# Performance work log

Measured on AMD Instinct MI355X. Metric: run time of the kernel, lower is better.

The kernel has to match this reference:

```python
import jax, jax.numpy as jnp
import numpy as np

INPUT_SIZE = 4096.0
SIGMA = 3
CONF_THR = 0.8
DIST_THR = (6 * SIGMA + 2) / 2.0  # 10.0, as in DecodeSPM.__init__
KP_DIST_THR = 2.0                 # hardcoded in forward's get_spm_keypoints call
MAX_ROOTS = 256                   # fixed cap on greedy NMS iterations (padded outputs)


def setup_inputs() -> dict:
    key = jax.random.key(0)
    x = jax.random.normal(key, (1, 35, 1024, 1024), dtype=jnp.float32)
    return {"x": x}


def _decode_spm(x):
    S = x.shape[-1]
    hm = jax.nn.sigmoid(x[0, 0])      # [S, S] root-joint heatmap (pred=True)
    disp = jnp.tanh(x[0, 1:])         # [2*Kp, S, S] displacement maps
    num_kp = disp.shape[0] // 2
    z = jnp.sqrt(jnp.asarray(2.0, x.dtype)) * S  # sqrt(S^2 + S^2)

    conf = hm.reshape(-1)             # [S*S]
    ii = jnp.arange(S * S)
    ys = (ii // S).astype(x.dtype)
    xs = (ii % S).astype(x.dtype)
    # candidates below conf threshold are permanently suppressed
    scores0 = jnp.where(conf > CONF_THR, conf, -jnp.inf)

    def step(scores, _):
        idx = jnp.argmax(scores)                      # highest remaining confidence
        valid = jnp.isfinite(scores[idx])
        cx, cy = xs[idx], ys[idx]
        d2 = (xs - cx) ** 2 + (ys - cy) ** 2
        # greedy suppression: drop everything within DIST_THR (incl. chosen point)
        scores = jnp.where(d2 <= DIST_THR ** 2, -jnp.inf, scores)
        return scores, (cx, cy, valid)

    _, (cxs, cys, valids) = jax.lax.scan(step, scores0, None, length=MAX_ROOTS)

    mask = valids.astype(x.dtype)                     # [R]
    root = jnp.stack([cxs, cys], axis=-1) * mask[:, None]   # [R, 2] (x, y)

    # gather displacement values at each root location: [2*Kp, R] -> [R, Kp, 2]
    yi = cys.astype(jnp.int32)
    xi = cxs.astype(jnp.int32)
    dvals = disp[:, yi, xi].T.reshape(MAX_ROOTS, num_kp, 2)  # (dx, dy) per kp

    kp = dvals * z + root[:, None, :]                  # [R, Kp, 2]
    d = jnp.sqrt(jnp.sum((kp - root[:, None, :]) ** 2, axis=-1, keepdims=True))
    kp = jnp.where(d < KP_DIST_THR, jnp.zeros_like(kp), kp) * mask[:, None, None]

    scale = INPUT_SIZE / S
    return root * scale, kp * scale, valids


def reference(x):
    # root_joints [MAX_ROOTS, 2], keypoints [MAX_ROOTS, Kp, 2], validity mask [MAX_ROOTS]
    return _decode_spm(x)
```

## Files before the change

kernel.cpp:

```cpp
#include <hip/hip_runtime.h>
#include <math.h>


#define SS 1024
#define MAXR 256
#define NBIN 16384
#define CAP 1024
#define TARGET 768u
#define B0 0x3F4CCCCEu
#define KEYB0 0xBF4CCCCEu
#define CONFL_MAX 8
#define CELL_CAP 8

struct WS {
  unsigned int hist[NBIN];
  unsigned int dstOff[NBIN];
  unsigned int cutBits;
  unsigned int candCount;
  int nValid;
  int pad0;
  int rootX[MAXR];
  int rootY[MAXR];
  unsigned long long cand[CAP];
};

__global__ __launch_bounds__(256) void spm_hist(const float* __restrict__ x,
                                                WS* __restrict__ w) {
  const int base = blockIdx.x << 10;
  const int tid = threadIdx.x;
#pragma unroll
  for (int j = 0; j < 4; ++j) {
    float v = x[base + tid + (j << 8)];
    float s = 1.0f / (1.0f + expf(-v));
    if (s > 0.8f) {
      unsigned int b = __float_as_uint(s);
      unsigned int bin = (b - B0) >> 8;
      if (bin > NBIN - 1) bin = NBIN - 1;
      atomicAdd(&w->hist[bin], 1u);
    }
  }
}

__global__ __launch_bounds__(1024) void spm_cut(WS* __restrict__ w) {
  __shared__ unsigned int sc[1024];
  __shared__ unsigned int cutBinSh;
  __shared__ unsigned int cnSh;
  const int t = threadIdx.x;
  const int base = t << 4;
  unsigned int cnt[16];
  unsigned int chunkSum = 0;
#pragma unroll
  for (int i = 0; i < 16; ++i) { cnt[i] = w->hist[base + i]; chunkSum += cnt[i]; }
  sc[t] = chunkSum;
  __syncthreads();
  for (int off = 1; off < 1024; off <<= 1) {
    unsigned int v = sc[t] + ((t + off < 1024) ? sc[t + off] : 0u);
    __syncthreads();
    sc[t] = v;
    __syncthreads();
  }
  const unsigned int tailBeyond = (t < 1023) ? sc[t + 1] : 0u;
  unsigned int run = tailBeyond;
  unsigned int sufL[16];
  for (int i = 15; i >= 0; --i) {
    w->dstOff[base + i] = run;
    run += cnt[i];
    sufL[i] = run;
  }
  if (t == 0) {
    cutBinSh = 0;
    unsigned int total = sufL[0];
    cnSh = (total < CAP) ? total : CAP;
  }
  __syncthreads();
#pragma unroll
  for (int i = 0; i < 16; ++i) {
    unsigned int nxt = (i < 15) ? sufL[i + 1] : tailBeyond;
    if (sufL[i] >= TARGET && nxt < TARGET) {
      cutBinSh = (unsigned)(base + i);
      cnSh = (sufL[i] < CAP) ? sufL[i] : CAP;
    }
  }
  __syncthreads();
  if (t == 0) {
    w->cutBits = B0 + (cutBinSh << 8);
    w->candCount = cnSh;
  }
}

__global__ __launch_bounds__(256) void spm_compact(const float* __restrict__ x,
                                                   WS* __restrict__ w) {
  const unsigned int cb = w->cutBits;
  const int base = blockIdx.x << 10;
  const int tid = threadIdx.x;
#pragma unroll
  for (int j = 0; j < 4; ++j) {
    int p = base + tid + (j << 8);
    float v = x[p];
    float s = 1.0f / (1.0f + expf(-v));
    if (s > 0.8f) {
      unsigned int b = __float_as_uint(s);
      if (b >= cb) {
        unsigned int bin = (b - B0) >> 8;
        if (bin > NBIN - 1) bin = NBIN - 1;
        unsigned int pos = atomicAdd(&w->dstOff[bin], 1u);
        if (pos < CAP)
          w->cand[pos] =
              ((unsigned long long)(b | 0x80000000u) << 32) | (unsigned int)(~p);
      }
    }
  }
}

__global__ __launch_bounds__(1024) void spm_walk(WS* __restrict__ w,
                                                 float* __restrict__ out) {
  __shared__ unsigned long long s[CAP];
  __shared__ unsigned short binA[CAP];
  __shared__ unsigned int pxy[CAP];
  __shared__ int cellCnt[1024];
  __shared__ unsigned short cellList[1024 * CELL_CAP];
  __shared__ unsigned short confl[CAP * CONFL_MAX];
  __shared__ unsigned char ccnt[CAP];
  __shared__ unsigned char state[CAP];
  __shared__ int scv[CAP];
  __shared__ unsigned int rootPid[MAXR];
  __shared__ int nVsh;
  __shared__ int undecSh;
  __shared__ int ovfSh;
  const int tid = threadIdx.x;
  unsigned int cn = w->candCount;
  if (cn > CAP) cn = CAP;
  if ((unsigned)tid < cn) {
    unsigned long long k = w->cand[tid];
    s[tid] = k;
    binA[tid] = (unsigned short)(((unsigned int)(k >> 32) - KEYB0) >> 8);
  } else {
    s[tid] = 0ULL;
    binA[tid] = 0xFFFFu;
  }
  if (tid == 0) ovfSh = 0;
  cellCnt[tid] = 0;
  __syncthreads();
  const bool isStart =
      ((unsigned)tid < cn) && (tid == 0 || binA[tid] != binA[tid - 1]);
  if (isStart) {
    const unsigned short mybin = binA[tid];
    int e = tid + 1;
    while (e < (int)cn && binA[e] == mybin) ++e;
    for (int j = tid + 1; j < e; ++j) {
      unsigned long long key = s[j];
      int i2 = j - 1;
      while (i2 >= tid && s[i2] < key) { s[i2 + 1] = s[i2]; --i2; }
      s[i2 + 1] = key;
    }
  }
  __syncthreads();
  int myx = 0, myy = 0;
  if ((unsigned)tid < cn) {
    unsigned int pid = ~(unsigned int)s[tid];
    myx = (int)(pid & 1023u);
    myy = (int)(pid >> 10);
    pxy[tid] = (unsigned int)myx | ((unsigned int)myy << 16);
    int cell = ((myy >> 5) << 5) | (myx >> 5);
    int pos = atomicAdd(&cellCnt[cell], 1);
    if (pos < CELL_CAP) cellList[cell * CELL_CAP + pos] = (unsigned short)tid;
    else ovfSh = 1;
  }
  __syncthreads();
  int nc = 0;
  if ((unsigned)tid < cn) {
    int cy0 = (myy >= 10) ? ((myy - 10) >> 5) : 0;
    int cy1 = (((myy + 10) < 1023) ? (myy + 10) : 1023) >> 5;
    int cx0 = (myx >= 10) ? ((myx - 10) >> 5) : 0;
    int cx1 = (((myx + 10) < 1023) ? (myx + 10) : 1023) >> 5;
    for (int cyc = cy0; cyc <= cy1; ++cyc) {
      for (int cxc = cx0; cxc <= cx1; ++cxc) {
        int cell = (cyc << 5) | cxc;
        int cnt2 = cellCnt[cell];
        if (cnt2 > CELL_CAP) cnt2 = CELL_CAP;
        for (int e = 0; e < cnt2; ++e) {
          int j = (int)cellList[cell * CELL_CAP + e];
          if (j < tid) {
            unsigned int p = pxy[j];
            int dx = myx - (int)(p & 0xFFFFu);
            int dy = myy - (int)(p >> 16);
            if (dx * dx + dy * dy <= 100) {
              if (nc < CONFL_MAX) confl[tid * CONFL_MAX + nc] = (unsigned short)j;
              ++nc;
            }
          }
        }
      }
    }
    if (nc > CONFL_MAX) ovfSh = 1;
  }
  ccnt[tid] = (unsigned char)((nc < CONFL_MAX) ? nc : CONFL_MAX);
  state[tid] = ((unsigned)tid < cn) ? ((nc == 0) ? (unsigned char)1
                                                 : (unsigned char)0)
                                    : (unsigned char)2;
  __syncthreads();
  if (ovfSh == 0) {
    unsigned char myst = state[tid];
    const int lbase = tid * CONFL_MAX;
    const int ncl = (int)ccnt[tid];
    for (;;) {
      if (tid == 0) undecSh = 0;
      __syncthreads();
      if (myst == 0) {
        bool anyAcc = false, allRej = true;
        for (int k = 0; k < ncl; ++k) {
          unsigned char st = state[confl[lbase + k]];
          anyAcc = anyAcc || (st == 1);
          allRej = allRej && (st == 2);
        }
        unsigned char ns = anyAcc ? (unsigned char)2
                                  : (allRej ? (unsigned char)1 : (unsigned char)0);
        if (ns != 0) state[tid] = ns;
        myst = ns;
      }
      unsigned long long b = __ballot(myst == 0);
      if ((tid & 63) == 0 && b != 0ULL) atomicAdd(&undecSh, (int)__popcll(b));
      __syncthreads();
      if (undecSh == 0) break;
    }
    scv[tid] = (myst == 1) ? 1 : 0;
    __syncthreads();
    for (int off = 1; off < 1024; off <<= 1) {
      int v = scv[tid] + ((tid >= off) ? scv[tid - off] : 0);
      __syncthreads();
      scv[tid] = v;
      __syncthreads();
    }
    if (myst == 1) {
      int pos = scv[tid] - 1;
      if (pos < MAXR) rootPid[pos] = ~(unsigned int)s[tid];
    }
    if (tid == 0) {
      int total = scv[CAP - 1];
      nVsh = (total < MAXR) ? total : MAXR;
    }
  } else {
    if (tid < 64) {
      const int lane = tid;
      int rx0 = 16384, ry0 = 16384, rx1 = 16384, ry1 = 16384;
      int rx2 = 16384, ry2 = 16384, rx3 = 16384, ry3 = 16384;
      int n = 0;
      unsigned long long kcur = (cn > 0) ? s[0] : 0ULL;
      for (unsigned int c = 0; c < cn && n < MAXR; ++c) {
        unsigned long long knext = (c + 1 < cn) ? s[c + 1] : 0ULL;
        if (!(kcur >> 63)) break;
        unsigned int pid = ~(unsigned int)kcur;
        int cx = (int)(pid & 1023u), cy = (int)(pid >> 10);
        int d0x = cx - rx0, d0y = cy - ry0;
        int d1x = cx - rx1, d1y = cy - ry1;
        int d2x = cx - rx2, d2y = cy - ry2;
        int d3x = cx - rx3, d3y = cy - ry3;
        int hit = (d0x * d0x + d0y * d0y <= 100) |
                  (d1x * d1x + d1y * d1y <= 100) |
                  (d2x * d2x + d2y * d2y <= 100) |
                  (d3x * d3x + d3y * d3y <= 100);
        if (!__any(hit)) {
          int sl = n >> 6, ll = n & 63;
          if (lane == ll) {
            if (sl == 0)      { rx0 = cx; ry0 = cy; }
            else if (sl == 1) { rx1 = cx; ry1 = cy; }
            else if (sl == 2) { rx2 = cx; ry2 = cy; }
            else              { rx3 = cx; ry3 = cy; }
          }
          if (lane == 0) rootPid[n] = pid;
          n++;
        }
        kcur = knext;
      }
      if (lane == 0) nVsh = n;
    }
  }
  __syncthreads();
  const int nv = nVsh;
  if (tid < MAXR) {
    const int valid = (tid < nv) ? 1 : 0;
    unsigned int pid = valid ? rootPid[tid] : 0u;
    int cx = (int)(pid & 1023u), cy = (int)(pid >> 10);
    out[2 * tid]     = valid ? (float)cx * 4.0f : 0.0f;
    out[2 * tid + 1] = valid ? (float)cy * 4.0f : 0.0f;
    out[9216 + tid]  = valid ? 1.0f : 0.0f;
    w->rootX[tid] = valid ? cx : 0;
    w->rootY[tid] = valid ? cy : 0;
  }
  if (tid == 0) w->nValid = nv;
}

__global__ __launch_bounds__(64) void spm_kp(const float* __restrict__ x,
                                             const WS* __restrict__ w,
                                             float* __restrict__ out) {
  const int r = blockIdx.x;
  const int lane = threadIdx.x;
  const int nv = w->nValid;
  const bool valid = r < nv;
  const int cx = w->rootX[r], cy = w->rootY[r];
  if (lane < 17) {
    float kpx = 0.0f, kpy = 0.0f;
    if (valid) {
      const float z = sqrtf(2.0f) * 1024.0f;
      size_t base = (size_t)(1 + 2 * lane) * 1048576u + (size_t)(cy << 10) + (size_t)cx;
      float dvx = tanhf(x[base]);
      float dvy = tanhf(x[base + 1048576u]);
      float cxf = (float)cx, cyf = (float)cy;
      float px = dvx * z + cxf;
      float py = dvy * z + cyf;
      float ddx = px - cxf, ddy = py - cyf;
      float d = sqrtf(ddx * ddx + ddy * ddy);
      if (d < 2.0f) { px = 0.0f; py = 0.0f; }
      kpx = px * 4.0f;
      kpy = py * 4.0f;
    }
    out[512 + r * 34 + 2 * lane]     = kpx;
    out[512 + r * 34 + 2 * lane + 1] = kpy;
  }
}

extern "C" void kernel_launch(void* const* d_in, const int* in_sizes, int n_in,
                              void* d_out, int out_size, void* d_ws, size_t ws_size,
                              hipStream_t stream) {
  const float* x = (const float*)d_in[0];
  float* out = (float*)d_out;
  WS* w = (WS*)d_ws;

  hipMemsetAsync(d_ws, 0, NBIN * sizeof(unsigned int), stream);
  spm_hist<<<1024, 256, 0, stream>>>(x, w);
  spm_cut<<<1, 1024, 0, stream>>>(w);
  spm_compact<<<1024, 256, 0, stream>>>(x, w);
  spm_walk<<<1, 1024, 0, stream>>>(w, out);
  spm_kp<<<MAXR, 64, 0, stream>>>(x, w, out);
}
```

Measured before the change: 198.5 us.

## Fuse decode pipeline into one cooperative kernel with grid-wide syncs

Replaces the memset and the five separate launches (histogram, cut, compact, walk, keypoint gather) with one cooperative kernel of 256 blocks of 1024 threads. Grid syncs separate the phases. Each thread keeps its sigmoid bit patterns in registers between the histogram and compaction phases, so the heatmap is not re-read or re-transformed. The aim is to remove launch gaps and one pass over memory. In exchange it adds several grid-wide barriers and needs every block resident at once with a large LDS footprint. If the cooperative launch fails, the old multi-kernel path runs instead.

```diff
diff --git a/kernel.cpp b/kernel.cpp
--- a/kernel.cpp
+++ b/kernel.cpp
@@ -1,4 +1,5 @@
 #include <hip/hip_runtime.h>
+#include <hip/hip_cooperative_groups.h>
 #include <math.h>
 
 
@@ -11,6 +12,8 @@
 #define KEYB0 0xBF4CCCCEu
 #define CONFL_MAX 8
 #define CELL_CAP 8
+
+namespace cg = cooperative_groups;
 
 struct WS {
   unsigned int hist[NBIN];
@@ -24,6 +27,308 @@
   unsigned long long cand[CAP];
 };
 
+__device__ __forceinline__ float sigm(float v) {
+  return 1.0f / (1.0f + expf(-v));
+}
+
+__global__ __launch_bounds__(1024) void spm_fused(const float* __restrict__ x,
+                                                  WS* __restrict__ w,
+                                                  float* __restrict__ out) {
+  cg::grid_group grid = cg::this_grid();
+  const int tid = threadIdx.x;
+  const int bid = blockIdx.x;
+  const int gtid = (bid << 10) + tid;
+
+  __shared__ unsigned int sc[1024];
+  __shared__ unsigned long long s[CAP];
+  __shared__ unsigned short binA[CAP];
+  __shared__ unsigned int pxy[CAP];
+  __shared__ int cellCnt[1024];
+  __shared__ unsigned short cellList[1024 * CELL_CAP];
+  __shared__ unsigned short confl[CAP * CONFL_MAX];
+  __shared__ unsigned char ccnt[CAP];
+  __shared__ unsigned char state[CAP];
+  __shared__ int scv[CAP];
+  __shared__ unsigned int rootPid[MAXR];
+  __shared__ int nVsh;
+  __shared__ int undecSh;
+  __shared__ int ovfSh;
+
+  if (gtid < NBIN) w->hist[gtid] = 0;
+  grid.sync();
+
+  unsigned int bb[4];
+#pragma unroll
+  for (int j = 0; j < 4; ++j) {
+    float v = x[(j << 18) + gtid];
+    float sg = sigm(v);
+    bb[j] = 0u;
+    if (sg > 0.8f) {
+      unsigned int b = __float_as_uint(sg);
+      bb[j] = b;
+      unsigned int bin = (b - B0) >> 8;
+      if (bin > NBIN - 1) bin = NBIN - 1;
+      atomicAdd(&w->hist[bin], 1u);
+    }
+  }
+  grid.sync();
+
+  if (bid == 0) {
+    const int t = tid;
+    const int base = t << 4;
+    unsigned int cnt[16];
+    unsigned int chunkSum = 0;
+#pragma unroll
+    for (int i = 0; i < 16; ++i) { cnt[i] = w->hist[base + i]; chunkSum += cnt[i]; }
+    sc[t] = chunkSum;
+    __syncthreads();
+    for (int off = 1; off < 1024; off <<= 1) {
+      unsigned int v = sc[t] + ((t + off < 1024) ? sc[t + off] : 0u);
+      __syncthreads();
+      sc[t] = v;
+      __syncthreads();
+    }
+    const unsigned int tailBeyond = (t < 1023) ? sc[t + 1] : 0u;
+    unsigned int run = tailBeyond;
+    unsigned int sufL[16];
+    for (int i = 15; i >= 0; --i) {
+      w->dstOff[base + i] = run;
+      run += cnt[i];
+      sufL[i] = run;
+    }
+    __shared__ unsigned int cutBinSh;
+    __shared__ unsigned int cnSh;
+    if (t == 0) {
+      cutBinSh = 0;
+      unsigned int total = sufL[0];
+      cnSh = (total < CAP) ? total : CAP;
+    }
+    __syncthreads();
+#pragma unroll
+    for (int i = 0; i < 16; ++i) {
+      unsigned int nxt = (i < 15) ? sufL[i + 1] : tailBeyond;
+      if (sufL[i] >= TARGET && nxt < TARGET) {
+        cutBinSh = (unsigned)(base + i);
+        cnSh = (sufL[i] < CAP) ? sufL[i] : CAP;
+      }
+    }
+    __syncthreads();
+    if (t == 0) {
+      w->cutBits = B0 + (cutBinSh << 8);
+      w->candCount = cnSh;
+    }
+  }
+  grid.sync();
+
+  {
+    const unsigned int cb = w->cutBits;
+#pragma unroll
+    for (int j = 0; j < 4; ++j) {
+      unsigned int b = bb[j];
+      if (b >= cb) {
+        int p = (j << 18) + gtid;
+        unsigned int bin = (b - B0) >> 8;
+        if (bin > NBIN - 1) bin = NBIN - 1;
+        unsigned int pos = atomicAdd(&w->dstOff[bin], 1u);
+        if (pos < CAP)
+          w->cand[pos] =
+              ((unsigned long long)(b | 0x80000000u) << 32) | (unsigned int)(~p);
+      }
+    }
+  }
+  grid.sync();
+
+  if (bid == 0) {
+    unsigned int cn = w->candCount;
+    if (cn > CAP) cn = CAP;
+    if ((unsigned)tid < cn) {
+      unsigned long long k = w->cand[tid];
+      s[tid] = k;
+      binA[tid] = (unsigned short)(((unsigned int)(k >> 32) - KEYB0) >> 8);
+    } else {
+      s[tid] = 0ULL;
+      binA[tid] = 0xFFFFu;
+    }
+    if (tid == 0) ovfSh = 0;
+    cellCnt[tid] = 0;
+    __syncthreads();
+    const bool isStart =
+        ((unsigned)tid < cn) && (tid == 0 || binA[tid] != binA[tid - 1]);
+    if (isStart) {
+      const unsigned short mybin = binA[tid];
+      int e = tid + 1;
+      while (e < (int)cn && binA[e] == mybin) ++e;
+      for (int j = tid + 1; j < e; ++j) {
+        unsigned long long key = s[j];
+        int i2 = j - 1;
+        while (i2 >= tid && s[i2] < key) { s[i2 + 1] = s[i2]; --i2; }
+        s[i2 + 1] = key;
+      }
+    }
+    __syncthreads();
+    int myx = 0, myy = 0;
+    if ((unsigned)tid < cn) {
+      unsigned int pid = ~(unsigned int)s[tid];
+      myx = (int)(pid & 1023u);
+      myy = (int)(pid >> 10);
+      pxy[tid] = (unsigned int)myx | ((unsigned int)myy << 16);
+      int cell = ((myy >> 5) << 5) | (myx >> 5);
+      int pos = atomicAdd(&cellCnt[cell], 1);
+      if (pos < CELL_CAP) cellList[cell * CELL_CAP + pos] = (unsigned short)tid;
+      else ovfSh = 1;
+    }
+    __syncthreads();
+    int nc = 0;
+    if ((unsigned)tid < cn) {
+      int cy0 = (myy >= 10) ? ((myy - 10) >> 5) : 0;
+      int cy1 = (((myy + 10) < 1023) ? (myy + 10) : 1023) >> 5;
+      int cx0 = (myx >= 10) ? ((myx - 10) >> 5) : 0;
+      int cx1 = (((myx + 10) < 1023) ? (myx + 10) : 1023) >> 5;
+      for (int cyc = cy0; cyc <= cy1; ++cyc) {
+        for (int cxc = cx0; cxc <= cx1; ++cxc) {
+          int cell = (cyc << 5) | cxc;
+          int cnt2 = cellCnt[cell];
+          if (cnt2 > CELL_CAP) cnt2 = CELL_CAP;
+          for (int e = 0; e < cnt2; ++e) {
+            int j = (int)cellList[cell * CELL_CAP + e];
+            if (j < tid) {
+              unsigned int p = pxy[j];
+              int dx = myx - (int)(p & 0xFFFFu);
+              int dy = myy - (int)(p >> 16);
+              if (dx * dx + dy * dy <= 100) {
+                if (nc < CONFL_MAX) confl[tid * CONFL_MAX + nc] = (unsigned short)j;
+                ++nc;
+              }
+            }
+          }
+        }
+      }
+      if (nc > CONFL_MAX) ovfSh = 1;
+    }
+    ccnt[tid] = (unsigned char)((nc < CONFL_MAX) ? nc : CONFL_MAX);
+    state[tid] = ((unsigned)tid < cn) ? ((nc == 0) ? (unsigned char)1
+                                                   : (unsigned char)0)
+                                      : (unsigned char)2;
+    __syncthreads();
+    if (ovfSh == 0) {
+      unsigned char myst = state[tid];
+      const int lbase = tid * CONFL_MAX;
+      const int ncl = (int)ccnt[tid];
+      for (;;) {
+        if (tid == 0) undecSh = 0;
+        __syncthreads();
+        if (myst == 0) {
+          bool anyAcc = false, allRej = true;
+          for (int k = 0; k < ncl; ++k) {
+            unsigned char st = state[confl[lbase + k]];
+            anyAcc = anyAcc || (st == 1);
+            allRej = allRej && (st == 2);
+          }
+          unsigned char ns = anyAcc ? (unsigned char)2
+                                    : (allRej ? (unsigned char)1 : (unsigned char)0);
+          if (ns != 0) state[tid] = ns;
+          myst = ns;
+        }
+        unsigned long long b = __ballot(myst == 0);
+        if ((tid & 63) == 0 && b != 0ULL) atomicAdd(&undecSh, (int)__popcll(b));
+        __syncthreads();
+        if (undecSh == 0) break;
+      }
+      scv[tid] = (myst == 1) ? 1 : 0;
+      __syncthreads();
+      for (int off = 1; off < 1024; off <<= 1) {
+        int v = scv[tid] + ((tid >= off) ? scv[tid - off] : 0);
+        __syncthreads();
+        scv[tid] = v;
+        __syncthreads();
+      }
+      if (myst == 1) {
+        int pos = scv[tid] - 1;
+        if (pos < MAXR) rootPid[pos] = ~(unsigned int)s[tid];
+      }
+      if (tid == 0) {
+        int total = scv[CAP - 1];
+        nVsh = (total < MAXR) ? total : MAXR;
+      }
+    } else {
+      if (tid < 64) {
+        const int lane = tid;
+        int rx0 = 16384, ry0 = 16384, rx1 = 16384, ry1 = 16384;
+        int rx2 = 16384, ry2 = 16384, rx3 = 16384, ry3 = 16384;
+        int n = 0;
+        unsigned long long kcur = (cn > 0) ? s[0] : 0ULL;
+        for (unsigned int c = 0; c < cn && n < MAXR; ++c) {
+          unsigned long long knext = (c + 1 < cn) ? s[c + 1] : 0ULL;
+          if (!(kcur >> 63)) break;
+          unsigned int pid = ~(unsigned int)kcur;
+          int cx = (int)(pid & 1023u), cy = (int)(pid >> 10);
+          int d0x = cx - rx0, d0y = cy - ry0;
+          int d1x = cx - rx1, d1y = cy - ry1;
+          int d2x = cx - rx2, d2y = cy - ry2;
+          int d3x = cx - rx3, d3y = cy - ry3;
+          int hit = (d0x * d0x + d0y * d0y <= 100) |
+                    (d1x * d1x + d1y * d1y <= 100) |
+                    (d2x * d2x + d2y * d2y <= 100) |
+                    (d3x * d3x + d3y * d3y <= 100);
+          if (!__any(hit)) {
+            int sl = n >> 6, ll = n & 63;
+            if (lane == ll) {
+              if (sl == 0)      { rx0 = cx; ry0 = cy; }
+              else if (sl == 1) { rx1 = cx; ry1 = cy; }
+              else if (sl == 2) { rx2 = cx; ry2 = cy; }
+              else              { rx3 = cx; ry3 = cy; }
+            }
+            if (lane == 0) rootPid[n] = pid;
+            n++;
+          }
+          kcur = knext;
+        }
+        if (lane == 0) nVsh = n;
+      }
+    }
+    __syncthreads();
+    const int nv = nVsh;
+    if (tid < MAXR) {
+      const int valid = (tid < nv) ? 1 : 0;
+      unsigned int pid = valid ? rootPid[tid] : 0u;
+      int cx = (int)(pid & 1023u), cy = (int)(pid >> 10);
+      out[2 * tid]     = valid ? (float)cx * 4.0f : 0.0f;
+      out[2 * tid + 1] = valid ? (float)cy * 4.0f : 0.0f;
+      out[9216 + tid]  = valid ? 1.0f : 0.0f;
+      w->rootX[tid] = valid ? cx : 0;
+      w->rootY[tid] = valid ? cy : 0;
+    }
+    if (tid == 0) w->nValid = nv;
+  }
+  grid.sync();
+
+  {
+    const int r = bid;
+    const int nv = w->nValid;
+    const bool valid = r < nv;
+    if (tid < 34) {
+      float kp = 0.0f;
+      const int k = tid >> 1;
+      const int coord = tid & 1;
+      if (valid) {
+        const int cx = w->rootX[r], cy = w->rootY[r];
+        const float z = sqrtf(2.0f) * 1024.0f;
+        size_t base = (size_t)(1 + 2 * k + coord) * 1048576u +
+                      (size_t)(cy << 10) + (size_t)cx;
+        float dv = tanhf(x[base]);
+        float cf = coord ? (float)cy : (float)cx;
+        float p = dv * z + cf;
+        float dd = p - cf;
+        float od = __shfl_xor(dd, 1);
+        float d = sqrtf(dd * dd + od * od);
+        if (d < 2.0f) p = 0.0f;
+        kp = p * 4.0f;
+      }
+      out[512 + r * 34 + tid] = kp;
+    }
+  }
+}
+
 __global__ __launch_bounds__(256) void spm_hist(const float* __restrict__ x,
                                                 WS* __restrict__ w) {
   const int base = blockIdx.x << 10;
@@ -31,7 +336,7 @@
 #pragma unroll
   for (int j = 0; j < 4; ++j) {
     float v = x[base + tid + (j << 8)];
-    float s = 1.0f / (1.0f + expf(-v));
+    float s = sigm(v);
     if (s > 0.8f) {
       unsigned int b = __float_as_uint(s);
       unsigned int bin = (b - B0) >> 8;
@@ -97,7 +402,7 @@
   for (int j = 0; j < 4; ++j) {
     int p = base + tid + (j << 8);
     float v = x[p];
-    float s = 1.0f / (1.0f + expf(-v));
+    float s = sigm(v);
     if (s > 0.8f) {
       unsigned int b = __float_as_uint(s);
       if (b >= cb) {
@@ -326,10 +631,15 @@
   float* out = (float*)d_out;
   WS* w = (WS*)d_ws;
 
-  hipMemsetAsync(d_ws, 0, NBIN * sizeof(unsigned int), stream);
-  spm_hist<<<1024, 256, 0, stream>>>(x, w);
-  spm_cut<<<1, 1024, 0, stream>>>(w);
-  spm_compact<<<1024, 256, 0, stream>>>(x, w);
-  spm_walk<<<1, 1024, 0, stream>>>(w, out);
-  spm_kp<<<MAXR, 64, 0, stream>>>(x, w, out);
-}
+  void* args[] = {(void*)&x, (void*)&w, (void*)&out};
+  hipError_t rc = hipLaunchCooperativeKernel((const void*)spm_fused, dim3(256),
+                                             dim3(1024), args, 0, stream);
+  if (rc != hipSuccess) {
+    hipMemsetAsync(d_ws, 0, NBIN * sizeof(unsigned int), stream);
+    spm_hist<<<1024, 256, 0, stream>>>(x, w);
+    spm_cut<<<1, 1024, 0, stream>>>(w);
+    spm_compact<<<1024, 256, 0, stream>>>(x, w);
+    spm_walk<<<1, 1024, 0, stream>>>(w, out);
+    spm_kp<<<MAXR, 64, 0, stream>>>(x, w, out);
+  }
+}
```

New measurement: 315.1 us. 1.59x slower.
